# Optimization experiments

Measured on AMD Instinct MI355X. Metric: run time of the kernel, lower is better.

## Reference

```python
import jax, jax.numpy as jnp
import numpy as np

B, T, INPUT_DIM = 4, 2048, 256
D_MODEL = 512                       # hidden_dim // 2
EXPAND = 2
D_INNER = D_MODEL * EXPAND          # 1024
HEADDIM = 128                       # _pick_headdim(1024)
NHEADS = D_INNER // HEADDIM         # 8
DSTATE = 16
DCONV = 4
NLAYERS = 4
CONV_DIM = D_INNER + 2 * DSTATE            # 1056
D_IN_PROJ = 2 * D_INNER + 2 * DSTATE + NHEADS  # 2088
EPS = 1e-5


def _dir_params(key):
    ks = jax.random.split(key, 5)
    return dict(
        in_w=jax.random.normal(ks[0], (NLAYERS, D_IN_PROJ, D_MODEL)) * 0.02,
        conv_w=jax.random.normal(ks[1], (NLAYERS, CONV_DIM, DCONV)) * 0.1,
        conv_b=jnp.zeros((NLAYERS, CONV_DIM)),
        dt_bias=jnp.log(jnp.expm1(jax.random.uniform(ks[2], (NLAYERS, NHEADS), minval=1e-3, maxval=0.1))),
        A_log=jnp.log(jax.random.uniform(ks[3], (NLAYERS, NHEADS), minval=1.0, maxval=16.0)),
        D=jnp.ones((NLAYERS, NHEADS)),
        rms_w=jnp.ones((NLAYERS, D_INNER)),
        out_w=jax.random.normal(ks[4], (NLAYERS, D_MODEL, D_INNER)) * 0.02,
    )


def setup_inputs():
    key = jax.random.key(0)
    kx, ke, kf, kb = jax.random.split(key, 4)
    inp = {
        "x": jax.random.normal(kx, (B, T, INPUT_DIM), dtype=jnp.float32),
        "embed_w": jax.random.normal(ke, (D_MODEL, INPUT_DIM)) * 0.02,
        "embed_b": jnp.zeros((D_MODEL,)),
        "ln1_w": jnp.ones((D_MODEL,)), "ln1_b": jnp.zeros((D_MODEL,)),
        "lnout_w": jnp.ones((2 * D_MODEL,)), "lnout_b": jnp.zeros((2 * D_MODEL,)),
    }
    for tag, p in (("f", _dir_params(kf)), ("b", _dir_params(kb))):
        for k, v in p.items():
            inp[f"{k}_{tag}"] = v
    return inp


def _silu(x):
    return x * jax.nn.sigmoid(x)


def _layernorm(x, w, b):
    m = jnp.mean(x, -1, keepdims=True)
    v = jnp.mean((x - m) ** 2, -1, keepdims=True)
    return (x - m) * jax.lax.rsqrt(v + EPS) * w + b


def _mamba2(h, in_w, conv_w, conv_b, dt_bias, A_log, Dh, rms_w, out_w):
    """One Mamba2 (SSD) block: in_proj -> causal depthwise conv -> selective scan
    -> gated RMSNorm -> out_proj. Sequential scan is math-equivalent to the
    chunked SSD kernel."""
    Bb, Tt, _ = h.shape
    zxbcdt = jnp.einsum('btd,ed->bte', h, in_w)
    z = zxbcdt[..., :D_INNER]
    xBC = zxbcdt[..., D_INNER:D_INNER + CONV_DIM]
    dt = zxbcdt[..., D_INNER + CONV_DIM:]                      # [B,T,H]
    # causal depthwise conv over time (kernel DCONV), then silu
    xc = jax.lax.conv_general_dilated(
        jnp.transpose(xBC, (0, 2, 1)), conv_w[:, None, :], (1,),
        [(DCONV - 1, 0)], feature_group_count=CONV_DIM)
    xBC = _silu(jnp.transpose(xc, (0, 2, 1)) + conv_b)
    xs = xBC[..., :D_INNER].reshape(Bb, Tt, NHEADS, HEADDIM)   # [B,T,H,P]
    Bm = xBC[..., D_INNER:D_INNER + DSTATE]                    # [B,T,N]
    Cm = xBC[..., D_INNER + DSTATE:]                           # [B,T,N]
    dt = jax.nn.softplus(dt + dt_bias)                         # [B,T,H]
    dA = jnp.exp(dt * (-jnp.exp(A_log)))                       # [B,T,H]
    xdt = xs * dt[..., None]                                   # [B,T,H,P]
    tm = lambda a: jnp.moveaxis(a, 1, 0)                       # time-major

    def step(s, inp):
        dA_t, xdt_t, B_t, C_t = inp
        s = dA_t[:, :, None, None] * s + xdt_t[..., None] * B_t[:, None, None, :]
        return s, jnp.einsum('bhpn,bn->bhp', s, C_t)

    s0 = jnp.zeros((Bb, NHEADS, HEADDIM, DSTATE), h.dtype)
    _, ys = jax.lax.scan(step, s0, (tm(dA), tm(xdt), tm(Bm), tm(Cm)))
    y = jnp.moveaxis(ys, 0, 1) + Dh[None, None, :, None] * xs
    y = y.reshape(Bb, Tt, D_INNER)
    g = y * _silu(z)                                           # gated RMSNorm (norm after gate)
    g = g * jax.lax.rsqrt(jnp.mean(g * g, -1, keepdims=True) + EPS) * rms_w
    return jnp.einsum('bti,oi->bto', g, out_w)


def _forward(x, embed_w, embed_b, ln1_w, ln1_b, lnout_w, lnout_b,
             in_w_f, conv_w_f, conv_b_f, dt_bias_f, A_log_f, D_f, rms_w_f, out_w_f,
             in_w_b, conv_w_b, conv_b_b, dt_bias_b, A_log_b, D_b, rms_w_b, out_w_b):
    h = _layernorm(jnp.einsum('bti,oi->bto', x, embed_w) + embed_b, ln1_w, ln1_b)
    h_f, h_b = h, h[:, ::-1]
    for i in range(NLAYERS):
        h_f = _mamba2(h_f, in_w_f[i], conv_w_f[i], conv_b_f[i], dt_bias_f[i],
                      A_log_f[i], D_f[i], rms_w_f[i], out_w_f[i]) + h_f
    for i in range(NLAYERS):
        h_b = _mamba2(h_b, in_w_b[i], conv_w_b[i], conv_b_b[i], dt_bias_b[i],
                      A_log_b[i], D_b[i], rms_w_b[i], out_w_b[i]) + h_b
    out = jnp.concatenate([h_f, h_b[:, ::-1]], axis=-1)        # [B,T,2*D_MODEL]
    return _layernorm(out, lnout_w, lnout_b)


def reference(x, embed_w, embed_b, ln1_w, ln1_b, lnout_w, lnout_b,
              in_w_f, conv_w_f, conv_b_f, dt_bias_f, A_log_f, D_f, rms_w_f, out_w_f,
              in_w_b, conv_w_b, conv_b_b, dt_bias_b, A_log_b, D_b, rms_w_b, out_w_b):
    return _forward(x, embed_w, embed_b, ln1_w, ln1_b, lnout_w, lnout_b,
                    in_w_f, conv_w_f, conv_b_f, dt_bias_f, A_log_f, D_f, rms_w_f, out_w_f,
                    in_w_b, conv_w_b, conv_b_b, dt_bias_b, A_log_b, D_b, rms_w_b, out_w_b)
```

## Files before the change

kernel.cpp:

```cpp
#include <hip/hip_runtime.h>
#include <hip/hip_bf16.h>
#include <math.h>

#define BB 4
#define TT 2048
#define BT 8192
#define DM 512
#define DI 1024
#define NH 8
#define HD 128
#define DS 16
#define CONVD 1056
#define DPROJ 2088
#define NL 4
#define NE 131072

typedef __hip_bfloat16 bf16;
typedef __attribute__((ext_vector_type(8))) short short8;
typedef __attribute__((ext_vector_type(4))) short short4v;
typedef __attribute__((ext_vector_type(4))) float f32x4;

#define AS_G __attribute__((address_space(1)))
#define AS_L __attribute__((address_space(3)))

static __device__ __forceinline__ float b2f_raw(short v){
  union { unsigned u; float f; } c; c.u = ((unsigned)(unsigned short)v) << 16; return c.f;
}
static __device__ __forceinline__ float u32_lo(unsigned u){
  union { unsigned u; float f; } c; c.u = u << 16; return c.f;
}
static __device__ __forceinline__ float u32_hi(unsigned u){
  union { unsigned u; float f; } c; c.u = u & 0xffff0000u; return c.f;
}
static __device__ __forceinline__ unsigned pack_bf16x2(float a, float b){
  unsigned lo = __bfloat16_as_ushort(__float2bfloat16(a));
  unsigned hi = __bfloat16_as_ushort(__float2bfloat16(b));
  return lo | (hi << 16);
}

static __device__ __forceinline__ void red2(float& a, float& b, float* sb){
  #pragma unroll
  for (int o = 32; o; o >>= 1){ a += __shfl_down(a, o); b += __shfl_down(b, o); }
  int w = threadIdx.x >> 6;
  if ((threadIdx.x & 63) == 0){ sb[w] = a; sb[4+w] = b; }
  __syncthreads();
  a = sb[0]+sb[1]+sb[2]+sb[3];
  b = sb[4]+sb[5]+sb[6]+sb[7];
}

__global__ __launch_bounds__(256) void detect_dtype(const void* x, int* flagp){
  __shared__ int cnt;
  if (threadIdx.x == 0) cnt = 0;
  __syncthreads();
  const bf16* p = (const bf16*)x;
  int bad = 0;
  for (int i = threadIdx.x; i < 32768; i += 256){
    float v = __bfloat162float(p[i]);
    if (!isfinite(v) || fabsf(v) > 1e4f) bad++;
  }
  atomicAdd(&cnt, bad);
  __syncthreads();
  if (threadIdx.x == 0) *flagp = (cnt > 100) ? 1 : 0;
}

__global__ __launch_bounds__(256) void convert_in(const void* src, bf16* dst, int n,
                                                  const int* flagp){
  int f = *flagp;
  for (int i = blockIdx.x*256 + threadIdx.x; i < n; i += gridDim.x*256){
    if (f) dst[i] = __float2bfloat16(((const float*)src)[i]);
    else   dst[i] = ((const bf16*)src)[i];
  }
}

template<int OP>
__global__ __launch_bounds__(256,4) void gemm_nt(
    const bf16* __restrict__ A, const bf16* __restrict__ W0, const bf16* __restrict__ W1,
    bf16* C, const bf16* X, float* aux,
    int M, int N, int K, int lda, long sA, long sC)
{
  const int z = blockIdx.z;
  const bf16* Az = A + (long)z * sA;
  const bf16* W = z ? W1 : W0;
  const int m0 = blockIdx.x * 128, n0 = blockIdx.y * 128;
  __shared__ __align__(16) bf16 As[2][128*32];
  __shared__ __align__(16) bf16 Bs[2][128*32];
  const int tid  = threadIdx.x;
  const int lane = tid & 63, wv = tid >> 6;
  const int wmB = (wv >> 1)*64;
  const int wnB = (wv & 1)*64;
  const int quad = lane >> 4, l16 = lane & 15;
  const int srow = lane >> 2;
  const int skb  = (((lane & 3) ^ ((srow >> 1) & 3)) * 16);
  const int rslot = ((quad ^ ((l16 >> 1) & 3)) * 16);

  f32x4 acc[4][4];
  #pragma unroll
  for (int i=0;i<4;i++)
    #pragma unroll
    for (int j=0;j<4;j++) acc[i][j] = (f32x4){0.f,0.f,0.f,0.f};

  auto stage = [&](int k0, int buf){
    #pragma unroll
    for (int is = 0; is < 2; ++is){
      int r = is*64 + wv*16 + srow;
      const char* gA = (const char*)(Az + (long)(m0 + r)*lda + k0) + skb;
      char* lA = (char*)(&As[buf][0]) + (long)(is*64 + wv*16)*64;
      __builtin_amdgcn_global_load_lds((const AS_G void*)gA, (AS_L void*)lA, 16, 0, 0);
    }
    #pragma unroll
    for (int is = 0; is < 2; ++is){
      int r = is*64 + wv*16 + srow;
      int rn = n0 + r; rn = rn < N ? rn : N-1;
      const char* gB = (const char*)(W + (long)rn*K + k0) + skb;
      char* lB = (char*)(&Bs[buf][0]) + (long)(is*64 + wv*16)*64;
      __builtin_amdgcn_global_load_lds((const AS_G void*)gB, (AS_L void*)lB, 16, 0, 0);
    }
  };
  auto compute = [&](int buf){
    short8 af[4], bfr[4];
    #pragma unroll
    for (int mi=0;mi<4;mi++)
      af[mi]  = *(const short8*)((const char*)&As[buf][0] + (long)(wmB+mi*16+l16)*64 + rslot);
    #pragma unroll
    for (int ni=0;ni<4;ni++)
      bfr[ni] = *(const short8*)((const char*)&Bs[buf][0] + (long)(wnB+ni*16+l16)*64 + rslot);
    #pragma unroll
    for (int mi=0;mi<4;mi++)
      #pragma unroll
      for (int ni=0;ni<4;ni++)
        acc[mi][ni] = __builtin_amdgcn_mfma_f32_16x16x32_bf16(af[mi], bfr[ni], acc[mi][ni], 0, 0, 0);
  };

  stage(0, 0);
  __syncthreads();
  for (int k0 = 0; k0 < K; k0 += 64){
    if (k0 + 32 < K) stage(k0 + 32, 1);
    compute(0);
    __syncthreads();
    if (k0 + 64 < K) stage(k0 + 64, 0);
    compute(1);
    __syncthreads();
  }

  bf16* Cz = C + (long)z * sC;
  const bf16* Xz = (OP==2) ? (X + (long)z * sC) : X;
  #pragma unroll
  for (int mi=0;mi<4;mi++){
    #pragma unroll
    for (int ni=0;ni<4;ni++){
      #pragma unroll
      for (int r=0;r<4;r++){
        int row = m0 + wmB + mi*16 + quad*4 + r;
        int col = n0 + wnB + ni*16 + l16;
        if (col < N){
          float v = acc[mi][ni][r];
          if (OP==1) v += __bfloat162float(X[col]);
          if (OP==2) v += __bfloat162float(Xz[(long)row*N + col]);
          Cz[(long)row*N + col] = __float2bfloat16(v);
          if (OP==3 && col >= DPROJ-8)
            aux[(long)z*BT*8 + (long)row*8 + (col-(DPROJ-8))] = v;
        }
      }
    }
  }
}

__global__ __launch_bounds__(256) void embed_ln(const bf16* __restrict__ hp,
    const bf16* __restrict__ w, const bf16* __restrict__ bb, bf16* __restrict__ h)
{
  __shared__ float sb[8];
  int bt = blockIdx.x; int b = bt >> 11, t = bt & 2047;
  const bf16* r = hp + (long)bt*DM;
  int c0 = threadIdx.x, c1 = threadIdx.x + 256;
  float v0 = __bfloat162float(r[c0]);
  float v1 = __bfloat162float(r[c1]);
  float s = v0+v1, ss = v0*v0+v1*v1;
  red2(s, ss, sb);
  float m = s / DM;
  float var = ss / DM - m*m;
  float rs = rsqrtf(fmaxf(var, 0.f) + 1e-5f);
  float a0 = (v0-m)*rs*__bfloat162float(w[c0]) + __bfloat162float(bb[c0]);
  float a1 = (v1-m)*rs*__bfloat162float(w[c1]) + __bfloat162float(bb[c1]);
  bf16* o0 = h + (long)bt*DM;
  bf16* o1 = h + ((long)BT + (long)b*TT + (TT-1-t)) * DM;
  o0[c0] = __float2bfloat16(a0); o0[c1] = __float2bfloat16(a1);
  o1[c0] = __float2bfloat16(a0); o1[c1] = __float2bfloat16(a1);
}

__global__ __launch_bounds__(256) void conv_silu(const bf16* __restrict__ zx,
    const bf16* __restrict__ cw0, const bf16* __restrict__ cw1,
    const bf16* __restrict__ cb0, const bf16* __restrict__ cb1,
    bf16* __restrict__ xbc)
{
  int bt = blockIdx.x, dir = blockIdx.y;
  int t = bt & 2047;
  const bf16* cw = dir ? cw1 : cw0;
  const bf16* cb = dir ? cb1 : cb0;
  const bf16* zr = zx + ((long)dir*BT + bt)*DPROJ + DI;
  bf16* orow = xbc + ((long)dir*BT + bt)*CONVD;
  for (int cg = threadIdx.x; cg < CONVD/4; cg += 256){
    int c = cg*4;
    short8 w01 = *(const short8*)(cw + c*4);
    short8 w23 = *(const short8*)(cw + c*4 + 8);
    short4v bi = *(const short4v*)(cb + c);
    float acc[4];
    #pragma unroll
    for (int k=0;k<4;k++) acc[k] = b2f_raw(bi[k]);
    #pragma unroll
    for (int j=0;j<4;j++){
      if (t - 3 + j >= 0){
        short4v xv = *(const short4v*)(zr + (long)(j-3)*DPROJ + c);
        acc[0] = fmaf(b2f_raw(w01[j]),   b2f_raw(xv[0]), acc[0]);
        acc[1] = fmaf(b2f_raw(w01[4+j]), b2f_raw(xv[1]), acc[1]);
        acc[2] = fmaf(b2f_raw(w23[j]),   b2f_raw(xv[2]), acc[2]);
        acc[3] = fmaf(b2f_raw(w23[4+j]), b2f_raw(xv[3]), acc[3]);
      }
    }
    short4v ov;
    #pragma unroll
    for (int k=0;k<4;k++){
      float sg = 1.f / (1.f + expf(-acc[k]));
      ov[k] = (short)__bfloat16_as_ushort(__float2bfloat16(acc[k] * sg));
    }
    *(short4v*)(orow + c) = ov;
  }
}

__global__ __launch_bounds__(256) void dt_kernel(const float* __restrict__ draw,
    const bf16* __restrict__ db0, const bf16* __restrict__ db1,
    const bf16* __restrict__ al0, const bf16* __restrict__ al1,
    float2* __restrict__ dadt)
{
  int idx = blockIdx.x*256 + threadIdx.x;
  int dir = idx >> 16, r = idx & 65535;
  int bt = r >> 3, h = r & 7;
  int b = bt >> 11, t = bt & 2047;
  float x = draw[idx] + __bfloat162float((dir?db1:db0)[h]);
  float sp = (x > 20.f) ? x : log1pf(expf(x));
  float a = expf(-expf(__bfloat162float((dir?al1:al0)[h])) * sp);
  long o = (((long)dir*BB + b)*NH + h)*TT + t;
  float2 v; v.x = a; v.y = sp;
  dadt[o] = v;
}

#define CLG_LOAD(G, T0) do{ \
  _Pragma("unroll") \
  for (int _i=0;_i<4;_i++){ \
    const bf16* _rr = xr + (long)((T0)+_i)*CONVD; \
    G##x[_i]  = *(const unsigned*)(_rr + xoff); \
    G##B0[_i] = *(const short8*)(_rr + DI); \
    G##B1[_i] = *(const short8*)(_rr + DI + 8); \
    G##d[_i]  = ddr[(T0)+_i]; \
  } }while(0)

#define CLG_STEP(G) do{ \
  _Pragma("unroll") \
  for (int _i=0;_i<4;_i++){ \
    float _da = G##d[_i].x, _dt = G##d[_i].y; \
    float _x0 = u32_lo(G##x[_i]), _x1 = u32_hi(G##x[_i]); \
    float _xd0 = _x0*_dt, _xd1 = _x1*_dt; \
    _Pragma("unroll") \
    for (int _n=0;_n<8;_n++){ \
      float _b = b2f_raw(G##B0[_i][_n]); \
      s0[_n] = fmaf(_da, s0[_n], _xd0*_b); \
      s1[_n] = fmaf(_da, s1[_n], _xd1*_b); \
      float _b2 = b2f_raw(G##B1[_i][_n]); \
      s0[8+_n] = fmaf(_da, s0[8+_n], _xd0*_b2); \
      s1[8+_n] = fmaf(_da, s1[8+_n], _xd1*_b2); \
    } \
    pacc *= _da; \
  } }while(0)

#define CAG_LOAD(G, T0) do{ \
  _Pragma("unroll") \
  for (int _i=0;_i<4;_i++){ \
    const bf16* _rr = xr + (long)((T0)+_i)*CONVD; \
    G##x[_i]  = *(const unsigned*)(_rr + xoff); \
    G##B0[_i] = *(const short8*)(_rr + DI); \
    G##B1[_i] = *(const short8*)(_rr + DI + 8); \
    G##C0[_i] = *(const short8*)(_rr + DI + DS); \
    G##C1[_i] = *(const short8*)(_rr + DI + DS + 8); \
    G##d[_i]  = ddr[(T0)+_i]; \
  } }while(0)

#define CAG_STEP(G, T0) do{ \
  _Pragma("unroll") \
  for (int _i=0;_i<4;_i++){ \
    float _da = G##d[_i].x, _dt = G##d[_i].y; \
    float _x0 = u32_lo(G##x[_i]), _x1 = u32_hi(G##x[_i]); \
    float _xd0 = _x0*_dt, _xd1 = _x1*_dt; \
    float _a0 = 0.f, _a1 = 0.f; \
    _Pragma("unroll") \
    for (int _n=0;_n<8;_n++){ \
      float _b = b2f_raw(G##B0[_i][_n]); \
      float _c = b2f_raw(G##C0[_i][_n]); \
      s0[_n] = fmaf(_da, s0[_n], _xd0*_b); \
      s1[_n] = fmaf(_da, s1[_n], _xd1*_b); \
      _a0 = fmaf(s0[_n], _c, _a0); \
      _a1 = fmaf(s1[_n], _c, _a1); \
      float _b2 = b2f_raw(G##B1[_i][_n]); \
      float _c2 = b2f_raw(G##C1[_i][_n]); \
      s0[8+_n] = fmaf(_da, s0[8+_n], _xd0*_b2); \
      s1[8+_n] = fmaf(_da, s1[8+_n], _xd1*_b2); \
      _a0 = fmaf(s0[8+_n], _c2, _a0); \
      _a1 = fmaf(s1[8+_n], _c2, _a1); \
    } \
    *(unsigned*)(xw + (long)((T0)+_i)*CONVD + xoff) = \
        pack_bf16x2(_a0 + Dv*_x0, _a1 + Dv*_x1); \
  } }while(0)

__global__ __launch_bounds__(256,1) void chunk_local(const bf16* __restrict__ xbc,
    const float2* __restrict__ dadt, float* __restrict__ SC, float* __restrict__ Pc,
    int cl, int nch)
{
  int c = blockIdx.x;
  int dbh = blockIdx.y*4 + (threadIdx.x >> 6);
  int lane = threadIdx.x & 63;
  int dir = dbh >> 5, b = (dbh >> 3) & 3, h = dbh & 7;
  const bf16* xr = xbc + ((long)dir*BT + (long)b*TT) * CONVD;
  const float2* ddr = dadt + (long)dbh*TT;
  const int xoff = h*HD + lane*2;
  float s0[16], s1[16];
  #pragma unroll
  for (int n=0;n<16;n++){ s0[n]=0.f; s1[n]=0.f; }
  float pacc = 1.f;
  const int c0 = c*cl;

  unsigned Ax[4], Bx[4]; short8 AB0[4], AB1[4], BB0[4], BB1[4]; float2 Ad[4], Bd[4];
  CLG_LOAD(A, c0);
  for (int t0 = c0; t0 < c0+cl; t0 += 8){
    CLG_LOAD(B, t0+4);
    CLG_STEP(A);
    if (t0+8 < c0+cl) CLG_LOAD(A, t0+8);
    CLG_STEP(B);
  }
  float* sc = SC + (long)c*NE + (long)dbh*2048 + lane*32;
  #pragma unroll
  for (int n=0;n<16;n++){ sc[n] = s0[n]; sc[16+n] = s1[n]; }
  if (lane == 0) Pc[dbh*nch + c] = pacc;
}

template<int NCH>
__global__ __launch_bounds__(256) void chunk_combine(float* __restrict__ SC,
    const float* __restrict__ Pc)
{
  int e = blockIdx.x*256 + threadIdx.x;
  int dbh = e >> 11;
  float s = 0.f;
  #pragma unroll
  for (int c=0;c<NCH;c++){
    float tmp = SC[(long)c*NE + e];
    SC[(long)c*NE + e] = s;
    s = Pc[dbh*NCH + c]*s + tmp;
  }
}

__global__ __launch_bounds__(256,1) void chunk_apply(bf16* __restrict__ xbc,
    const float2* __restrict__ dadt, const float* __restrict__ SC,
    const bf16* __restrict__ D0, const bf16* __restrict__ D1, int cl)
{
  int c = blockIdx.x;
  int dbh = blockIdx.y*4 + (threadIdx.x >> 6);
  int lane = threadIdx.x & 63;
  int dir = dbh >> 5, b = (dbh >> 3) & 3, h = dbh & 7;
  const bf16* xr = xbc + ((long)dir*BT + (long)b*TT) * CONVD;
  bf16* xw = xbc + ((long)dir*BT + (long)b*TT) * CONVD;
  const float2* ddr = dadt + (long)dbh*TT;
  const int xoff = h*HD + lane*2;
  float Dv = __bfloat162float(dir ? D1[h] : D0[h]);
  const float* sc = SC + (long)c*NE + (long)dbh*2048 + lane*32;
  float s0[16], s1[16];
  #pragma unroll
  for (int n=0;n<16;n++){ s0[n] = sc[n]; s1[n] = sc[16+n]; }
  const int c0 = c*cl;

  unsigned Ax[4], Bx[4];
  short8 AB0[4], AB1[4], BB0[4], BB1[4], AC0[4], AC1[4], BC0[4], BC1[4];
  float2 Ad[4], Bd[4];
  CAG_LOAD(A, c0);
  for (int t0 = c0; t0 < c0+cl; t0 += 8){
    CAG_LOAD(B, t0+4);
    CAG_STEP(A, t0);
    if (t0+8 < c0+cl) CAG_LOAD(A, t0+8);
    CAG_STEP(B, t0+4);
  }
}

__global__ __launch_bounds__(256) void gate_rms(const bf16* __restrict__ xbc, bf16* zx,
    const bf16* __restrict__ rw0, const bf16* __restrict__ rw1)
{
  __shared__ float sb[8];
  int bt = blockIdx.x, dir = blockIdx.y;
  const bf16* yr = xbc + ((long)dir*BT + bt)*CONVD;
  bf16* zr = zx + ((long)dir*BT + bt)*DPROJ;
  const bf16* rw = dir ? rw1 : rw0;
  int c = threadIdx.x*4;
  short4v yv4 = *(const short4v*)(yr + c);
  short4v zv4 = *(const short4v*)(zr + c);
  short4v rw4 = *(const short4v*)(rw + c);
  float gv[4], ss = 0.f, dummy = 0.f;
  #pragma unroll
  for (int k=0;k<4;k++){
    float yv = b2f_raw(yv4[k]);
    float zv = b2f_raw(zv4[k]);
    float sg = 1.f/(1.f+expf(-zv));
    gv[k] = yv * zv * sg;
    ss += gv[k]*gv[k];
  }
  red2(ss, dummy, sb);
  float sc = rsqrtf(ss / DI + 1e-5f);
  short4v ov;
  #pragma unroll
  for (int k=0;k<4;k++)
    ov[k] = (short)__bfloat16_as_ushort(__float2bfloat16(gv[k]*sc*b2f_raw(rw4[k])));
  *(short4v*)(zr + c) = ov;
}

__global__ __launch_bounds__(256) void final_ln(const bf16* __restrict__ h,
    const bf16* __restrict__ lw, const bf16* __restrict__ lb, void* out,
    int mode, const int* flagp)
{
  __shared__ float sb[8];
  int bt = blockIdx.x; int b = bt >> 11, t = bt & 2047;
  int f32out = mode ? *flagp : 0;
  const bf16* rf = h + (long)bt*DM;
  const bf16* rb = h + ((long)BT + (long)b*TT + (TT-1-t))*DM;
  float v[4], s = 0.f, ss = 0.f;
  #pragma unroll
  for (int i=0;i<4;i++){
    int c = threadIdx.x + i*256;
    v[i] = __bfloat162float(c < DM ? rf[c] : rb[c-DM]);
    s += v[i]; ss += v[i]*v[i];
  }
  red2(s, ss, sb);
  float m = s / (2*DM);
  float var = ss / (2*DM) - m*m;
  float rs = rsqrtf(fmaxf(var, 0.f) + 1e-5f);
  #pragma unroll
  for (int i=0;i<4;i++){
    int c = threadIdx.x + i*256;
    float o = (v[i]-m)*rs*__bfloat162float(lw[c]) + __bfloat162float(lb[c]);
    if (f32out) ((float*)out)[(long)bt*(2*DM) + c] = o;
    else        ((bf16*)out)[(long)bt*(2*DM) + c] = __float2bfloat16(o);
  }
}

extern "C" void kernel_launch(void* const* d_in, const int* in_sizes, int n_in,
                              void* d_out, int out_size, void* d_ws, size_t ws_size,
                              hipStream_t stream)
{
  char* wsp = (char*)d_ws;
  auto take = [&](size_t bytes){ char* p = wsp; wsp += (bytes + 63) & ~(size_t)63; return p; };
  int*   flagp = (int*)  take(4);
  bf16*  h     = (bf16*) take((size_t)2*BT*DM*2);
  bf16*  zx    = (bf16*) take((size_t)2*BT*DPROJ*2);
  bf16*  xbc   = (bf16*) take((size_t)2*BT*CONVD*2);
  float2* dadt = (float2*)take((size_t)2*BB*NH*TT*8);
  float* draw  = (float*)take((size_t)2*BT*NH*4);
  float* Pc    = (float*)take((size_t)64*64*4);
  char* preCanon = wsp;

  static const int cnt[23] = {
    BT*256, DM*256, DM, DM, DM, 2*DM, 2*DM,
    NL*DPROJ*DM, NL*CONVD*4, NL*CONVD, NL*NH, NL*NH, NL*NH, NL*DI, NL*DM*DI,
    NL*DPROJ*DM, NL*CONVD*4, NL*CONVD, NL*NH, NL*NH, NL*NH, NL*DI, NL*DM*DI };
  bf16* canon[23];
  for (int i = 0; i < 23; ++i) canon[i] = (bf16*)take((size_t)cnt[i]*2);
  char* postCanon = wsp;

  const size_t scUnit = (size_t)NE*4;
  size_t usedFull   = (size_t)(postCanon - (char*)d_ws);
  size_t usedDirect = (size_t)(preCanon  - (char*)d_ws);
  int convMode, NCHR; float* SC;
  if      (ws_size >= usedFull + 64*scUnit){ convMode=1; NCHR=64; SC=(float*)postCanon; }
  else if (ws_size >= usedFull + 32*scUnit){ convMode=1; NCHR=32; SC=(float*)postCanon; }
  else if (ws_size >= usedFull + 16*scUnit){ convMode=1; NCHR=16; SC=(float*)postCanon; }
  else {
    convMode = 0;
    if      (ws_size >= usedDirect + 64*scUnit) NCHR=64;
    else if (ws_size >= usedDirect + 32*scUnit) NCHR=32;
    else                                        NCHR=16;
    SC = (float*)preCanon;
  }
  const int CLR = TT / NCHR;

  const bf16* in[23];
  if (convMode){
    detect_dtype<<<1,256,0,stream>>>(d_in[0], flagp);
    for (int i = 0; i < 23; ++i){
      int grid = (cnt[i] + 255)/256; if (grid > 2048) grid = 2048;
      convert_in<<<grid,256,0,stream>>>(d_in[i], canon[i], cnt[i], flagp);
      in[i] = canon[i];
    }
  } else {
    for (int i = 0; i < 23; ++i) in[i] = (const bf16*)d_in[i];
  }

  const bf16* x       = in[0];
  const bf16* embed_w = in[1];
  const bf16* embed_b = in[2];
  const bf16* ln1_w   = in[3];
  const bf16* ln1_b   = in[4];
  const bf16* lnout_w = in[5];
  const bf16* lnout_b = in[6];
  const bf16* in_w[2]   = {in[7],  in[15]};
  const bf16* conv_w[2] = {in[8],  in[16]};
  const bf16* conv_b[2] = {in[9],  in[17]};
  const bf16* dt_b[2]   = {in[10], in[18]};
  const bf16* A_log[2]  = {in[11], in[19]};
  const bf16* Dp[2]     = {in[12], in[20]};
  const bf16* rms_w[2]  = {in[13], in[21]};
  const bf16* out_w[2]  = {in[14], in[22]};

  bf16* hpre = xbc;

  gemm_nt<1><<<dim3(64,4,1),256,0,stream>>>(x, embed_w, embed_w, hpre, embed_b, nullptr,
                                            BT, DM, 256, 256, 0, 0);
  embed_ln<<<dim3(BT),256,0,stream>>>(hpre, ln1_w, ln1_b, h);

  for (int i = 0; i < NL; ++i){
    gemm_nt<3><<<dim3(64,17,2),256,0,stream>>>(h, in_w[0]+(size_t)i*DPROJ*DM, in_w[1]+(size_t)i*DPROJ*DM,
        zx, nullptr, draw, BT, DPROJ, DM, DM, (long)BT*DM, (long)BT*DPROJ);
    conv_silu<<<dim3(BT,2),256,0,stream>>>(zx, conv_w[0]+(size_t)i*CONVD*4, conv_w[1]+(size_t)i*CONVD*4,
        conv_b[0]+(size_t)i*CONVD, conv_b[1]+(size_t)i*CONVD, xbc);
    dt_kernel<<<dim3(512),256,0,stream>>>(draw, dt_b[0]+i*NH, dt_b[1]+i*NH,
        A_log[0]+i*NH, A_log[1]+i*NH, dadt);
    chunk_local<<<dim3(NCHR,16),256,0,stream>>>(xbc, dadt, SC, Pc, CLR, NCHR);
    if      (NCHR == 64) chunk_combine<64><<<dim3(NE/256),256,0,stream>>>(SC, Pc);
    else if (NCHR == 32) chunk_combine<32><<<dim3(NE/256),256,0,stream>>>(SC, Pc);
    else                 chunk_combine<16><<<dim3(NE/256),256,0,stream>>>(SC, Pc);
    chunk_apply<<<dim3(NCHR,16),256,0,stream>>>(xbc, dadt, SC, Dp[0]+i*NH, Dp[1]+i*NH, CLR);
    gate_rms<<<dim3(BT,2),256,0,stream>>>(xbc, zx, rms_w[0]+(size_t)i*DI, rms_w[1]+(size_t)i*DI);
    gemm_nt<2><<<dim3(64,4,2),256,0,stream>>>(zx, out_w[0]+(size_t)i*DM*DI, out_w[1]+(size_t)i*DM*DI,
        h, h, nullptr, BT, DM, DI, DPROJ, (long)BT*DPROJ, (long)BT*DM);
  }

  final_ln<<<dim3(BT),256,0,stream>>>(h, lnout_w, lnout_b, d_out, convMode, flagp);
  (void)in_sizes; (void)n_in; (void)out_size;
}
```

Measured before the change: 1.210 ms.

## Fuse chunk scan output with gated RMSNorm into one kernel

Merges chunk_apply and gate_rms into a single kernel in which each 512-thread block covers all 8 heads of one (dir, batch) chunk. The RMS sum over the full 1024-wide row is reduced through wave shuffles and shared memory, and the gated, normalised output goes straight into zx. This drops the y write to xbc, its re-read, and one kernel launch per layer. In exchange it adds two block barriers every 4 timesteps and removes the double-buffered software prefetch of B/C/x loads, so the scan is more exposed to load latency.

```diff
diff --git a/kernel.cpp b/kernel.cpp
--- a/kernel.cpp
+++ b/kernel.cpp
@@ -271,44 +271,6 @@
     pacc *= _da; \
   } }while(0)
 
-#define CAG_LOAD(G, T0) do{ \
-  _Pragma("unroll") \
-  for (int _i=0;_i<4;_i++){ \
-    const bf16* _rr = xr + (long)((T0)+_i)*CONVD; \
-    G##x[_i]  = *(const unsigned*)(_rr + xoff); \
-    G##B0[_i] = *(const short8*)(_rr + DI); \
-    G##B1[_i] = *(const short8*)(_rr + DI + 8); \
-    G##C0[_i] = *(const short8*)(_rr + DI + DS); \
-    G##C1[_i] = *(const short8*)(_rr + DI + DS + 8); \
-    G##d[_i]  = ddr[(T0)+_i]; \
-  } }while(0)
-
-#define CAG_STEP(G, T0) do{ \
-  _Pragma("unroll") \
-  for (int _i=0;_i<4;_i++){ \
-    float _da = G##d[_i].x, _dt = G##d[_i].y; \
-    float _x0 = u32_lo(G##x[_i]), _x1 = u32_hi(G##x[_i]); \
-    float _xd0 = _x0*_dt, _xd1 = _x1*_dt; \
-    float _a0 = 0.f, _a1 = 0.f; \
-    _Pragma("unroll") \
-    for (int _n=0;_n<8;_n++){ \
-      float _b = b2f_raw(G##B0[_i][_n]); \
-      float _c = b2f_raw(G##C0[_i][_n]); \
-      s0[_n] = fmaf(_da, s0[_n], _xd0*_b); \
-      s1[_n] = fmaf(_da, s1[_n], _xd1*_b); \
-      _a0 = fmaf(s0[_n], _c, _a0); \
-      _a1 = fmaf(s1[_n], _c, _a1); \
-      float _b2 = b2f_raw(G##B1[_i][_n]); \
-      float _c2 = b2f_raw(G##C1[_i][_n]); \
-      s0[8+_n] = fmaf(_da, s0[8+_n], _xd0*_b2); \
-      s1[8+_n] = fmaf(_da, s1[8+_n], _xd1*_b2); \
-      _a0 = fmaf(s0[8+_n], _c2, _a0); \
-      _a1 = fmaf(s1[8+_n], _c2, _a1); \
-    } \
-    *(unsigned*)(xw + (long)((T0)+_i)*CONVD + xoff) = \
-        pack_bf16x2(_a0 + Dv*_x0, _a1 + Dv*_x1); \
-  } }while(0)
-
 __global__ __launch_bounds__(256,1) void chunk_local(const bf16* __restrict__ xbc,
     const float2* __restrict__ dadt, float* __restrict__ SC, float* __restrict__ Pc,
     int cl, int nch)
@@ -355,65 +317,93 @@
   }
 }
 
-__global__ __launch_bounds__(256,1) void chunk_apply(bf16* __restrict__ xbc,
+__global__ __launch_bounds__(512,2) void chunk_apply_gate(
+    const bf16* __restrict__ xbc, bf16* __restrict__ zx,
     const float2* __restrict__ dadt, const float* __restrict__ SC,
-    const bf16* __restrict__ D0, const bf16* __restrict__ D1, int cl)
-{
+    const bf16* __restrict__ D0, const bf16* __restrict__ D1,
+    const bf16* __restrict__ rw0, const bf16* __restrict__ rw1, int cl)
+{
+  __shared__ float sb[8][4];
   int c = blockIdx.x;
-  int dbh = blockIdx.y*4 + (threadIdx.x >> 6);
+  int db = blockIdx.y;
+  int dir = db >> 2, b = db & 3;
+  int h = threadIdx.x >> 6;
   int lane = threadIdx.x & 63;
-  int dir = dbh >> 5, b = (dbh >> 3) & 3, h = dbh & 7;
+  int dbh = dir*32 + b*8 + h;
   const bf16* xr = xbc + ((long)dir*BT + (long)b*TT) * CONVD;
-  bf16* xw = xbc + ((long)dir*BT + (long)b*TT) * CONVD;
+  bf16* zrow = zx + ((long)dir*BT + (long)b*TT) * DPROJ;
   const float2* ddr = dadt + (long)dbh*TT;
   const int xoff = h*HD + lane*2;
   float Dv = __bfloat162float(dir ? D1[h] : D0[h]);
+  const bf16* rw = dir ? rw1 : rw0;
+  float rwl = __bfloat162float(rw[xoff]);
+  float rwh = __bfloat162float(rw[xoff+1]);
   const float* sc = SC + (long)c*NE + (long)dbh*2048 + lane*32;
   float s0[16], s1[16];
   #pragma unroll
   for (int n=0;n<16;n++){ s0[n] = sc[n]; s1[n] = sc[16+n]; }
   const int c0 = c*cl;
 
-  unsigned Ax[4], Bx[4];
-  short8 AB0[4], AB1[4], BB0[4], BB1[4], AC0[4], AC1[4], BC0[4], BC1[4];
-  float2 Ad[4], Bd[4];
-  CAG_LOAD(A, c0);
-  for (int t0 = c0; t0 < c0+cl; t0 += 8){
-    CAG_LOAD(B, t0+4);
-    CAG_STEP(A, t0);
-    if (t0+8 < c0+cl) CAG_LOAD(A, t0+8);
-    CAG_STEP(B, t0+4);
-  }
-}
-
-__global__ __launch_bounds__(256) void gate_rms(const bf16* __restrict__ xbc, bf16* zx,
-    const bf16* __restrict__ rw0, const bf16* __restrict__ rw1)
-{
-  __shared__ float sb[8];
-  int bt = blockIdx.x, dir = blockIdx.y;
-  const bf16* yr = xbc + ((long)dir*BT + bt)*CONVD;
-  bf16* zr = zx + ((long)dir*BT + bt)*DPROJ;
-  const bf16* rw = dir ? rw1 : rw0;
-  int c = threadIdx.x*4;
-  short4v yv4 = *(const short4v*)(yr + c);
-  short4v zv4 = *(const short4v*)(zr + c);
-  short4v rw4 = *(const short4v*)(rw + c);
-  float gv[4], ss = 0.f, dummy = 0.f;
-  #pragma unroll
-  for (int k=0;k<4;k++){
-    float yv = b2f_raw(yv4[k]);
-    float zv = b2f_raw(zv4[k]);
-    float sg = 1.f/(1.f+expf(-zv));
-    gv[k] = yv * zv * sg;
-    ss += gv[k]*gv[k];
-  }
-  red2(ss, dummy, sb);
-  float sc = rsqrtf(ss / DI + 1e-5f);
-  short4v ov;
-  #pragma unroll
-  for (int k=0;k<4;k++)
-    ov[k] = (short)__bfloat16_as_ushort(__float2bfloat16(gv[k]*sc*b2f_raw(rw4[k])));
-  *(short4v*)(zr + c) = ov;
+  for (int t0 = c0; t0 < c0+cl; t0 += 4){
+    float gl[4], gh[4], sum2[4];
+    #pragma unroll
+    for (int i=0;i<4;i++){
+      const bf16* rr = xr + (long)(t0+i)*CONVD;
+      unsigned xv = *(const unsigned*)(rr + xoff);
+      short8 B0 = *(const short8*)(rr + DI);
+      short8 B1 = *(const short8*)(rr + DI + 8);
+      short8 C0 = *(const short8*)(rr + DI + DS);
+      short8 C1 = *(const short8*)(rr + DI + DS + 8);
+      unsigned zv = *(const unsigned*)(zrow + (long)(t0+i)*DPROJ + xoff);
+      float2 dd = ddr[t0+i];
+      float da = dd.x, dt = dd.y;
+      float x0 = u32_lo(xv), x1 = u32_hi(xv);
+      float xd0 = x0*dt, xd1 = x1*dt;
+      float a0 = 0.f, a1 = 0.f;
+      #pragma unroll
+      for (int n=0;n<8;n++){
+        float bb0 = b2f_raw(B0[n]), cc0 = b2f_raw(C0[n]);
+        s0[n] = fmaf(da, s0[n], xd0*bb0);
+        s1[n] = fmaf(da, s1[n], xd1*bb0);
+        a0 = fmaf(s0[n], cc0, a0);
+        a1 = fmaf(s1[n], cc0, a1);
+        float bb1 = b2f_raw(B1[n]), cc1 = b2f_raw(C1[n]);
+        s0[8+n] = fmaf(da, s0[8+n], xd0*bb1);
+        s1[8+n] = fmaf(da, s1[8+n], xd1*bb1);
+        a0 = fmaf(s0[8+n], cc1, a0);
+        a1 = fmaf(s1[8+n], cc1, a1);
+      }
+      float y0 = a0 + Dv*x0, y1 = a1 + Dv*x1;
+      float z0 = u32_lo(zv), z1 = u32_hi(zv);
+      float g0 = y0 * z0 * (1.f/(1.f+expf(-z0)));
+      float g1 = y1 * z1 * (1.f/(1.f+expf(-z1)));
+      gl[i] = g0; gh[i] = g1;
+      sum2[i] = g0*g0 + g1*g1;
+    }
+    #pragma unroll
+    for (int o=32;o;o>>=1){
+      #pragma unroll
+      for (int i=0;i<4;i++) sum2[i] += __shfl_down(sum2[i], o);
+    }
+    if (lane == 0){
+      #pragma unroll
+      for (int i=0;i<4;i++) sb[h][i] = sum2[i];
+    }
+    __syncthreads();
+    float scl[4];
+    #pragma unroll
+    for (int i=0;i<4;i++){
+      float tot = 0.f;
+      #pragma unroll
+      for (int w=0;w<8;w++) tot += sb[w][i];
+      scl[i] = rsqrtf(tot*(1.f/DI) + 1e-5f);
+    }
+    __syncthreads();
+    #pragma unroll
+    for (int i=0;i<4;i++)
+      *(unsigned*)(zrow + (long)(t0+i)*DPROJ + xoff) =
+          pack_bf16x2(gl[i]*scl[i]*rwl, gh[i]*scl[i]*rwh);
+  }
 }
 
 __global__ __launch_bounds__(256) void final_ln(const bf16* __restrict__ h,
@@ -529,8 +519,8 @@
     if      (NCHR == 64) chunk_combine<64><<<dim3(NE/256),256,0,stream>>>(SC, Pc);
     else if (NCHR == 32) chunk_combine<32><<<dim3(NE/256),256,0,stream>>>(SC, Pc);
     else                 chunk_combine<16><<<dim3(NE/256),256,0,stream>>>(SC, Pc);
-    chunk_apply<<<dim3(NCHR,16),256,0,stream>>>(xbc, dadt, SC, Dp[0]+i*NH, Dp[1]+i*NH, CLR);
-    gate_rms<<<dim3(BT,2),256,0,stream>>>(xbc, zx, rms_w[0]+(size_t)i*DI, rms_w[1]+(size_t)i*DI);
+    chunk_apply_gate<<<dim3(NCHR,8),512,0,stream>>>(xbc, zx, dadt, SC,
+        Dp[0]+i*NH, Dp[1]+i*NH, rms_w[0]+(size_t)i*DI, rms_w[1]+(size_t)i*DI, CLR);
     gemm_nt<2><<<dim3(64,4,2),256,0,stream>>>(zx, out_w[0]+(size_t)i*DM*DI, out_w[1]+(size_t)i*DM*DI,
         h, h, nullptr, BT, DM, DI, DPROJ, (long)BT*DPROJ, (long)BT*DM);
   }
```

Result: no change. 1.224 ms (+1.2%).
